# Performance work log

Hardware: AMD Instinct MI355X
Metric: run time of the kernel (lower is better)

The kernel has to match this reference:

```python
import jax, jax.numpy as jnp
import numpy as np

N_NODES = 75000
N_EDGES = 1200000
IN_FEATS = 64
OUT_FEATS = 64


def setup_inputs() -> dict:
    key = jax.random.key(0)
    k1, k2, k3, k4, k5 = jax.random.split(key, 5)
    feature = jax.random.normal(k1, (N_NODES, IN_FEATS), dtype=jnp.float32)
    src = jax.random.randint(k2, (N_EDGES,), 0, N_NODES, dtype=jnp.int32)
    dst = jax.random.randint(k3, (N_EDGES,), 0, N_NODES, dtype=jnp.int32)
    # degree: in-degree + 1 (clamped >= 1 so sqrt/div are well-defined), float32 node data
    deg = np.bincount(np.asarray(dst), minlength=N_NODES).astype(np.float32) + 1.0
    degree = jnp.asarray(deg)
    W = jax.random.normal(k4, (IN_FEATS, OUT_FEATS), dtype=jnp.float32) * (1.0 / np.sqrt(IN_FEATS))
    b = jax.random.normal(k5, (OUT_FEATS,), dtype=jnp.float32) * 0.01
    return {"feature": feature, "degree": degree, "src": src, "dst": dst, "W": W, "b": b}


def reference(feature, degree, src, dst, W, b):
    # message: m_e = h[src_e] / sqrt(degree[src_e])   -> [E, F]
    inv_sqrt_deg = 1.0 / jnp.sqrt(degree)
    m = feature[src] * inv_sqrt_deg[src][:, None]
    # reduce: sum messages into destination nodes      -> [N, F]
    agg = jax.ops.segment_sum(m, dst, num_segments=feature.shape[0])
    # node apply: h = (agg / sqrt(degree)) @ W + b     -> [N, O]
    h = agg * inv_sqrt_deg[:, None]
    return h @ W + b
```

## Files before the change

### kernel.cpp

```cpp
#include <hip/hip_runtime.h>

#define FEATS 64
#define PSZ   64
#define MAXP  1280
#define PSCH  1172
#define SPT   512
#define PEPT  3
#define CAPP  2560

typedef __attribute__((ext_vector_type(8))) short short8;
typedef __attribute__((ext_vector_type(4))) float floatx4;

static __device__ __forceinline__ unsigned short f2bf(float f) {
    const unsigned int u = __float_as_uint(f);
    return (unsigned short)((u + 0x7FFFu + ((u >> 16) & 1u)) >> 16);
}
static __device__ __forceinline__ float bflo(unsigned int u) {
    return __uint_as_float(u << 16);
}
static __device__ __forceinline__ float bfhi(unsigned int u) {
    return __uint_as_float(u & 0xFFFF0000u);
}

__global__ __launch_bounds__(SPT) void prep_scatter(
        const float* __restrict__ degree,
        const float* __restrict__ feature,
        const float* __restrict__ Wm,
        const int* __restrict__ src,
        const int* __restrict__ dst,
        unsigned short* __restrict__ Fs16,
        unsigned short* __restrict__ WtB,
        int* __restrict__ slab,
        unsigned short* __restrict__ runoff,
        int n_nodes, int n_edges, int np, int rows_per) {
    __shared__ int cnt[MAXP];
    __shared__ int swt[8];
    __shared__ __align__(16) int sval[PSCH];
    const int tid = threadIdx.x;
    const int lane = tid & 63;
    const int wv = tid >> 6;
    const int b = blockIdx.x;

    for (int i = tid; i < np; i += SPT) cnt[i] = 0;

    {
        const int r0 = b * rows_per;
        const int r1 = min(r0 + rows_per, n_nodes);
        const float4* f4 = (const float4*)feature;
        uint4* o4 = (uint4*)Fs16;
        for (int ch = r0 * 8 + tid; ch < r1 * 8; ch += SPT) {
            const float w = rsqrtf(degree[ch >> 3]);
            const float4 fa = f4[ch * 2];
            const float4 fb = f4[ch * 2 + 1];
            uint4 o;
            o.x = (unsigned int)f2bf(fa.x * w) | ((unsigned int)f2bf(fa.y * w) << 16);
            o.y = (unsigned int)f2bf(fa.z * w) | ((unsigned int)f2bf(fa.w * w) << 16);
            o.z = (unsigned int)f2bf(fb.x * w) | ((unsigned int)f2bf(fb.y * w) << 16);
            o.w = (unsigned int)f2bf(fb.z * w) | ((unsigned int)f2bf(fb.w * w) << 16);
            o4[ch] = o;
        }
        if (b == 0) {
            if (tid < FEATS) Fs16[(size_t)n_nodes * FEATS + tid] = 0;
            for (int idx = tid; idx < FEATS * FEATS; idx += SPT) {
                const int k = idx >> 6, n = idx & 63;
                WtB[n * FEATS + k] = f2bf(Wm[idx]);
            }
        }
    }
    __syncthreads();

    const int estart = b * PSCH;
    const int eend = min(estart + PSCH, n_edges);
    const int mb = eend - estart;

    int prk[PEPT];
#pragma unroll
    for (int k = 0; k < PEPT; ++k) {
        const int e = estart + tid + k * SPT;
        prk[k] = 0;
        if (e < eend) {
            const int d = dst[e];
            const int p = d >> 6;
            const int r = atomicAdd(&cnt[p], 1);
            prk[k] = p | (r << 11) | ((d & 63) << 23);
        }
    }
    __syncthreads();

    int my[3];
    int psum = 0;
    const int p0 = tid * 3;
#pragma unroll
    for (int j = 0; j < 3; ++j) {
        const int p = p0 + j;
        my[j] = psum;
        if (p < np) psum += cnt[p];
    }
    int x = psum;
#pragma unroll
    for (int off = 1; off < 64; off <<= 1) {
        const int v = __shfl_up(x, off);
        if (lane >= off) x += v;
    }
    if (lane == 63) swt[wv] = x;
    __syncthreads();
    int wbase = 0;
#pragma unroll
    for (int w = 0; w < 8; ++w) if (w < wv) wbase += swt[w];
    const int tbase = wbase + (x - psum);
#pragma unroll
    for (int j = 0; j < 3; ++j) {
        const int p = p0 + j;
        if (p < np) cnt[p] = tbase + my[j];
    }
    __syncthreads();

#pragma unroll
    for (int k = 0; k < PEPT; ++k) {
        const int e = estart + tid + k * SPT;
        if (e < eend) {
            const int pr = prk[k];
            const int p = pr & 2047;
            const int r = (pr >> 11) & 4095;
            const int dl = (pr >> 23) & 63;
            sval[cnt[p] + r] = (src[e] & 0x1FFFF) | (dl << 17);
        }
    }
    __syncthreads();

    int* so = slab + estart;
    const int m4 = mb >> 2;
    int4* so4 = (int4*)so;
    const int4* sv4 = (const int4*)sval;
    for (int i = tid; i < m4; i += SPT) so4[i] = sv4[i];
    for (int i = (m4 << 2) + tid; i < mb; i += SPT) so[i] = sval[i];
    unsigned short* ro = runoff + (size_t)b * (np + 1);
    for (int i = tid; i <= np; i += SPT)
        ro[i] = (unsigned short)((i < np) ? cnt[i] : mb);
}

__global__ __launch_bounds__(512, 8) void gather_apply6(
        const int* __restrict__ slab,
        const unsigned short* __restrict__ runoff,
        const float* __restrict__ degree,
        const unsigned short* __restrict__ Fs16,
        const unsigned short* __restrict__ WtB,
        const float* __restrict__ bias,
        float* __restrict__ out,
        int n_nodes, int np, int nbs) {
    __shared__ __align__(16) int ledges[CAPP];
    __shared__ __align__(16) unsigned short saggb[PSZ * 72];
    __shared__ int boffA[PSZ + 1];
    __shared__ int bcur[PSZ];
    __shared__ float swinv[PSZ];

    const int tid = threadIdx.x;
    const int lane = tid & 63;
    const int wv = tid >> 6;
    const int p = blockIdx.x;
    const int n0 = p * PSZ;
    const int nn = min(PSZ, n_nodes - n0);

    if (tid < PSZ) bcur[tid] = 0;
    if (wv == 0) {
        const float dg = (lane < nn) ? degree[n0 + lane] : 1.0f;
        swinv[lane] = rsqrtf(dg);
        const int c = (lane < nn) ? ((int)(dg + 0.5f) - 1) : 0;
        const int cp = (c + 15) & ~15;
        int x = cp;
#pragma unroll
        for (int off = 1; off < 64; off <<= 1) {
            const int v = __shfl_up(x, off);
            if (lane >= off) x += v;
        }
        if (lane == 0) boffA[0] = 0;
        boffA[lane + 1] = x;
    }
    __syncthreads();
    const int mpad = boffA[PSZ];

    if (mpad <= CAPP) {
        for (int i = tid; i < mpad; i += SPT) ledges[i] = n_nodes;
        __syncthreads();
        for (int rr = tid; rr < nbs; rr += SPT) {
            const unsigned short* ro = runoff + (size_t)rr * (np + 1);
            const int st = ro[p];
            const int en = ro[p + 1];
            const int* g = slab + (size_t)rr * PSCH;
            for (int q = st; q < en; ++q) {
                const int rec = g[q];
                const int dl = (rec >> 17) & 63;
                const int pos = boffA[dl] + atomicAdd(&bcur[dl], 1);
                ledges[pos] = rec & 0x1FFFF;
            }
        }
        __syncthreads();

        const int q8 = lane >> 3;
        const int c8 = lane & 7;
        const uint4* FsU4 = (const uint4*)Fs16;
        for (int n = wv; n < PSZ; n += 8) {
            const int st = boffA[n];
            const int en16 = boffA[n + 1];
            float a0 = 0.f, a1 = 0.f, a2 = 0.f, a3 = 0.f;
            float a4 = 0.f, a5 = 0.f, a6 = 0.f, a7 = 0.f;
#pragma unroll 2
            for (int j = st; j < en16; j += 16) {
                const int r0 = ledges[j + q8];
                const int r1 = ledges[j + 8 + q8];
                const uint4 u0 = FsU4[((size_t)r0 << 3) + c8];
                const uint4 u1 = FsU4[((size_t)r1 << 3) + c8];
                a0 += bflo(u0.x); a1 += bfhi(u0.x);
                a2 += bflo(u0.y); a3 += bfhi(u0.y);
                a4 += bflo(u0.z); a5 += bfhi(u0.z);
                a6 += bflo(u0.w); a7 += bfhi(u0.w);
                a0 += bflo(u1.x); a1 += bfhi(u1.x);
                a2 += bflo(u1.y); a3 += bfhi(u1.y);
                a4 += bflo(u1.z); a5 += bfhi(u1.z);
                a6 += bflo(u1.w); a7 += bfhi(u1.w);
            }
#define FOLD(v) v += __shfl_xor(v, 8); v += __shfl_xor(v, 16); v += __shfl_xor(v, 32)
            FOLD(a0); FOLD(a1); FOLD(a2); FOLD(a3);
            FOLD(a4); FOLD(a5); FOLD(a6); FOLD(a7);
#undef FOLD
            if (q8 == 0) {
                uint4 o;
                o.x = (unsigned int)f2bf(a0) | ((unsigned int)f2bf(a1) << 16);
                o.y = (unsigned int)f2bf(a2) | ((unsigned int)f2bf(a3) << 16);
                o.z = (unsigned int)f2bf(a4) | ((unsigned int)f2bf(a5) << 16);
                o.w = (unsigned int)f2bf(a6) | ((unsigned int)f2bf(a7) << 16);
                *(uint4*)(saggb + n * 72 + c8 * 8) = o;
            }
        }
    } else {
        __syncthreads();
        __syncthreads();
        for (int n = wv; n < PSZ; n += 8) {
            float acc = 0.f;
            for (int t = 0; t < nbs; ++t) {
                const unsigned short* ro = runoff + (size_t)t * (np + 1);
                const int gb = t * PSCH;
                const int e0 = ro[p + 1];
                for (int i = ro[p]; i < e0; ++i) {
                    const int rec = slab[gb + i];
                    if (((rec >> 17) & 63) == n) {
                        const unsigned int us =
                            Fs16[((size_t)(rec & 0x1FFFF) << 6) + lane];
                        acc += __uint_as_float(us << 16);
                    }
                }
            }
            saggb[n * 72 + lane] = f2bf(acc);
        }
    }
    __syncthreads();

    const int col = lane & 15;
    const int quad = lane >> 4;
    const int mt = wv >> 1;
    const int nh = (wv & 1) << 1;
    floatx4 acc[2] = {};
#pragma unroll
    for (int kt = 0; kt < 2; ++kt) {
        const short8 af = *(const short8*)(saggb + (mt * 16 + col) * 72 + kt * 32 + quad * 8);
#pragma unroll
        for (int t = 0; t < 2; ++t) {
            const int nt = nh + t;
            const short8 bf = *(const short8*)((const short*)WtB + (nt * 16 + col) * FEATS + kt * 32 + quad * 8);
            acc[t] = __builtin_amdgcn_mfma_f32_16x16x32_bf16(af, bf, acc[t], 0, 0, 0);
        }
    }
#pragma unroll
    for (int t = 0; t < 2; ++t) {
        const int nt = nh + t;
        const float bv = bias[nt * 16 + col];
#pragma unroll
        for (int r = 0; r < 4; ++r) {
            const int row = mt * 16 + quad * 4 + r;
            if (row < nn)
                out[(size_t)(n0 + row) * FEATS + nt * 16 + col] = swinv[row] * acc[t][r] + bv;
        }
    }
}

static inline size_t align256(size_t x) { return (x + 255) & ~(size_t)255; }

extern "C" void kernel_launch(void* const* d_in, const int* in_sizes, int n_in,
                              void* d_out, int out_size, void* d_ws, size_t ws_size,
                              hipStream_t stream) {
    const float* feature = (const float*)d_in[0];
    const float* degree  = (const float*)d_in[1];
    const int*   src     = (const int*)d_in[2];
    const int*   dst     = (const int*)d_in[3];
    const float* Wm      = (const float*)d_in[4];
    const float* bias    = (const float*)d_in[5];
    float* out = (float*)d_out;

    const int n_nodes = in_sizes[1];
    const int n_edges = in_sizes[2];
    const int np = (n_nodes + PSZ - 1) / PSZ;
    const int nbs = (n_edges + PSCH - 1) / PSCH;
    const int rows_per = (n_nodes + nbs - 1) / nbs;

    char* ws = (char*)d_ws;
    unsigned short* Fs16 = (unsigned short*)ws; ws += align256(((size_t)n_nodes + 1) * FEATS * 2);
    unsigned short* WtB  = (unsigned short*)ws; ws += align256((size_t)FEATS * FEATS * 2);
    int* slab = (int*)ws;                       ws += align256((size_t)nbs * PSCH * 4);
    unsigned short* runoff = (unsigned short*)ws; ws += align256((size_t)nbs * (np + 1) * 2);

    prep_scatter<<<nbs, SPT, 0, stream>>>(degree, feature, Wm, src, dst,
                                          Fs16, WtB, slab, runoff,
                                          n_nodes, n_edges, np, rows_per);
    gather_apply6<<<np, SPT, 0, stream>>>(slab, runoff, degree, Fs16, WtB, bias, out,
                                          n_nodes, np, nbs);
}
```

Baseline: 134.8 us.

## Split feature conversion into own kernel, enlarge edge chunks, transpose run offsets

Moves the feature-to-bf16 conversion and W transpose into a separate grid-stride kernel. The edge-bucketing kernel now handles four times as many edges per block, cutting the number of chunks each gather block has to scan. Run offsets are stored transposed so a gather block reads its per-chunk ranges contiguously, and two threads now share each chunk. Gather blocks are also remapped so neighbouring partitions land on the same XCD. The cost is an extra kernel launch and larger LDS use per sort block, which may lower its occupancy.

```diff
diff --git a/kernel.cpp b/kernel.cpp
--- a/kernel.cpp
+++ b/kernel.cpp
@@ -3,9 +3,9 @@
 #define FEATS 64
 #define PSZ   64
 #define MAXP  1280
-#define PSCH  1172
+#define PSCH  4688
 #define SPT   512
-#define PEPT  3
+#define PEPT  10
 #define CAPP  2560
 
 typedef __attribute__((ext_vector_type(8))) short short8;
@@ -22,17 +22,43 @@
     return __uint_as_float(u & 0xFFFF0000u);
 }
 
-__global__ __launch_bounds__(SPT) void prep_scatter(
+__global__ __launch_bounds__(256) void convert_k(
         const float* __restrict__ degree,
         const float* __restrict__ feature,
         const float* __restrict__ Wm,
+        unsigned short* __restrict__ Fs16,
+        unsigned short* __restrict__ WtB,
+        int n_nodes) {
+    const int gtid = blockIdx.x * 256 + threadIdx.x;
+    const int total = n_nodes * 8;
+    const float4* f4 = (const float4*)feature;
+    uint4* o4 = (uint4*)Fs16;
+    for (int ch = gtid; ch < total; ch += 2048 * 256) {
+        const float w = rsqrtf(degree[ch >> 3]);
+        const float4 fa = f4[ch * 2];
+        const float4 fb = f4[ch * 2 + 1];
+        uint4 o;
+        o.x = (unsigned int)f2bf(fa.x * w) | ((unsigned int)f2bf(fa.y * w) << 16);
+        o.y = (unsigned int)f2bf(fa.z * w) | ((unsigned int)f2bf(fa.w * w) << 16);
+        o.z = (unsigned int)f2bf(fb.x * w) | ((unsigned int)f2bf(fb.y * w) << 16);
+        o.w = (unsigned int)f2bf(fb.z * w) | ((unsigned int)f2bf(fb.w * w) << 16);
+        o4[ch] = o;
+    }
+    if (blockIdx.x == 0) {
+        if (threadIdx.x < FEATS) Fs16[(size_t)n_nodes * FEATS + threadIdx.x] = 0;
+        for (int idx = threadIdx.x; idx < FEATS * FEATS; idx += 256) {
+            const int k = idx >> 6, n = idx & 63;
+            WtB[n * FEATS + k] = f2bf(Wm[idx]);
+        }
+    }
+}
+
+__global__ __launch_bounds__(SPT) void prep_sort(
         const int* __restrict__ src,
         const int* __restrict__ dst,
-        unsigned short* __restrict__ Fs16,
-        unsigned short* __restrict__ WtB,
         int* __restrict__ slab,
-        unsigned short* __restrict__ runoff,
-        int n_nodes, int n_edges, int np, int rows_per) {
+        unsigned short* __restrict__ runoffT,
+        int n_edges, int np, int nbs) {
     __shared__ int cnt[MAXP];
     __shared__ int swt[8];
     __shared__ __align__(16) int sval[PSCH];
@@ -42,31 +68,6 @@
     const int b = blockIdx.x;
 
     for (int i = tid; i < np; i += SPT) cnt[i] = 0;
-
-    {
-        const int r0 = b * rows_per;
-        const int r1 = min(r0 + rows_per, n_nodes);
-        const float4* f4 = (const float4*)feature;
-        uint4* o4 = (uint4*)Fs16;
-        for (int ch = r0 * 8 + tid; ch < r1 * 8; ch += SPT) {
-            const float w = rsqrtf(degree[ch >> 3]);
-            const float4 fa = f4[ch * 2];
-            const float4 fb = f4[ch * 2 + 1];
-            uint4 o;
-            o.x = (unsigned int)f2bf(fa.x * w) | ((unsigned int)f2bf(fa.y * w) << 16);
-            o.y = (unsigned int)f2bf(fa.z * w) | ((unsigned int)f2bf(fa.w * w) << 16);
-            o.z = (unsigned int)f2bf(fb.x * w) | ((unsigned int)f2bf(fb.y * w) << 16);
-            o.w = (unsigned int)f2bf(fb.z * w) | ((unsigned int)f2bf(fb.w * w) << 16);
-            o4[ch] = o;
-        }
-        if (b == 0) {
-            if (tid < FEATS) Fs16[(size_t)n_nodes * FEATS + tid] = 0;
-            for (int idx = tid; idx < FEATS * FEATS; idx += SPT) {
-                const int k = idx >> 6, n = idx & 63;
-                WtB[n * FEATS + k] = f2bf(Wm[idx]);
-            }
-        }
-    }
     __syncthreads();
 
     const int estart = b * PSCH;
@@ -82,7 +83,7 @@
             const int d = dst[e];
             const int p = d >> 6;
             const int r = atomicAdd(&cnt[p], 1);
-            prk[k] = p | (r << 11) | ((d & 63) << 23);
+            prk[k] = p | (r << 11) | ((d & 63) << 24);
         }
     }
     __syncthreads();
@@ -121,8 +122,8 @@
         if (e < eend) {
             const int pr = prk[k];
             const int p = pr & 2047;
-            const int r = (pr >> 11) & 4095;
-            const int dl = (pr >> 23) & 63;
+            const int r = (pr >> 11) & 8191;
+            const int dl = (pr >> 24) & 63;
             sval[cnt[p] + r] = (src[e] & 0x1FFFF) | (dl << 17);
         }
     }
@@ -134,14 +135,13 @@
     const int4* sv4 = (const int4*)sval;
     for (int i = tid; i < m4; i += SPT) so4[i] = sv4[i];
     for (int i = (m4 << 2) + tid; i < mb; i += SPT) so[i] = sval[i];
-    unsigned short* ro = runoff + (size_t)b * (np + 1);
     for (int i = tid; i <= np; i += SPT)
-        ro[i] = (unsigned short)((i < np) ? cnt[i] : mb);
-}
-
-__global__ __launch_bounds__(512, 8) void gather_apply6(
+        runoffT[(size_t)i * nbs + b] = (unsigned short)((i < np) ? cnt[i] : mb);
+}
+
+__global__ __launch_bounds__(512, 8) void gather_apply7(
         const int* __restrict__ slab,
-        const unsigned short* __restrict__ runoff,
+        const unsigned short* __restrict__ runoffT,
         const float* __restrict__ degree,
         const unsigned short* __restrict__ Fs16,
         const unsigned short* __restrict__ WtB,
@@ -157,7 +157,14 @@
     const int tid = threadIdx.x;
     const int lane = tid & 63;
     const int wv = tid >> 6;
-    const int p = blockIdx.x;
+
+    int p;
+    {
+        const int bid = blockIdx.x;
+        const int q = np >> 3, r = np & 7;
+        const int xcd = bid & 7, idx = bid >> 3;
+        p = ((xcd < r) ? xcd * (q + 1) : r * (q + 1) + (xcd - r) * q) + idx;
+    }
     const int n0 = p * PSZ;
     const int nn = min(PSZ, n_nodes - n0);
 
@@ -182,12 +189,12 @@
     if (mpad <= CAPP) {
         for (int i = tid; i < mpad; i += SPT) ledges[i] = n_nodes;
         __syncthreads();
-        for (int rr = tid; rr < nbs; rr += SPT) {
-            const unsigned short* ro = runoff + (size_t)rr * (np + 1);
-            const int st = ro[p];
-            const int en = ro[p + 1];
+        for (int t = tid; t < nbs * 2; t += SPT) {
+            const int rr = t >> 1, sub = t & 1;
+            const int st = runoffT[(size_t)p * nbs + rr];
+            const int en = runoffT[(size_t)(p + 1) * nbs + rr];
             const int* g = slab + (size_t)rr * PSCH;
-            for (int q = st; q < en; ++q) {
+            for (int q = st + sub; q < en; q += 2) {
                 const int rec = g[q];
                 const int dl = (rec >> 17) & 63;
                 const int pos = boffA[dl] + atomicAdd(&bcur[dl], 1);
@@ -238,10 +245,10 @@
         for (int n = wv; n < PSZ; n += 8) {
             float acc = 0.f;
             for (int t = 0; t < nbs; ++t) {
-                const unsigned short* ro = runoff + (size_t)t * (np + 1);
+                const int st = runoffT[(size_t)p * nbs + t];
+                const int en = runoffT[(size_t)(p + 1) * nbs + t];
                 const int gb = t * PSCH;
-                const int e0 = ro[p + 1];
-                for (int i = ro[p]; i < e0; ++i) {
+                for (int i = st; i < en; ++i) {
                     const int rec = slab[gb + i];
                     if (((rec >> 17) & 63) == n) {
                         const unsigned int us =
@@ -300,17 +307,15 @@
     const int n_edges = in_sizes[2];
     const int np = (n_nodes + PSZ - 1) / PSZ;
     const int nbs = (n_edges + PSCH - 1) / PSCH;
-    const int rows_per = (n_nodes + nbs - 1) / nbs;
 
     char* ws = (char*)d_ws;
     unsigned short* Fs16 = (unsigned short*)ws; ws += align256(((size_t)n_nodes + 1) * FEATS * 2);
     unsigned short* WtB  = (unsigned short*)ws; ws += align256((size_t)FEATS * FEATS * 2);
     int* slab = (int*)ws;                       ws += align256((size_t)nbs * PSCH * 4);
-    unsigned short* runoff = (unsigned short*)ws; ws += align256((size_t)nbs * (np + 1) * 2);
-
-    prep_scatter<<<nbs, SPT, 0, stream>>>(degree, feature, Wm, src, dst,
-                                          Fs16, WtB, slab, runoff,
-                                          n_nodes, n_edges, np, rows_per);
-    gather_apply6<<<np, SPT, 0, stream>>>(slab, runoff, degree, Fs16, WtB, bias, out,
+    unsigned short* runoffT = (unsigned short*)ws; ws += align256((size_t)(np + 1) * nbs * 2);
+
+    convert_k<<<2048, 256, 0, stream>>>(degree, feature, Wm, Fs16, WtB, n_nodes);
+    prep_sort<<<nbs, SPT, 0, stream>>>(src, dst, slab, runoffT, n_edges, np, nbs);
+    gather_apply7<<<np, SPT, 0, stream>>>(slab, runoffT, degree, Fs16, WtB, bias, out,
                                           n_nodes, np, nbs);
 }
```

After: 133.1 us. About the same (-1.3%).
